# Kernel tuning notes

Hardware: AMD Instinct MI355X
Metric: run time of the kernel (lower is better)

Reference implementation:

```python
import jax, jax.numpy as jnp
import numpy as np

T, INP, HID, OUT = 32768, 1024, 1024, 7


def setup_inputs() -> dict:
    key = jax.random.key(0)
    ks = jax.random.split(key, 7)
    s_i = 1.0 / np.sqrt(INP)
    s_h = 1.0 / np.sqrt(2 * HID)
    s_o = 1.0 / np.sqrt(HID)
    return {
        "uterance": jax.random.normal(ks[0], (T, INP), dtype=jnp.float32),
        "Wi": jax.random.uniform(ks[1], (HID, INP), jnp.float32, -s_i, s_i),
        "bi": jax.random.uniform(ks[2], (HID,), jnp.float32, -s_i, s_i),
        "Wh": jax.random.uniform(ks[3], (HID, 2 * HID), jnp.float32, -s_h, s_h),
        "bh": jax.random.uniform(ks[4], (HID,), jnp.float32, -s_h, s_h),
        "Wo": jax.random.uniform(ks[5], (OUT, HID), jnp.float32, -s_o, s_o),
        "bo": jax.random.uniform(ks[6], (OUT,), jnp.float32, -s_o, s_o),
    }


def reference(uterance, Wi, bi, Wh, bh, Wo, bo):
    # Input projection is independent of the recurrence -> batch it once.
    # hidden_cur[t] = tanh(i2h(x_t)), shape [T, HID]
    hc_all = jnp.tanh(uterance @ Wi.T + bi)
    # Split h2h weight by the concat halves: combined = [prev, cur]
    Wh_prev = Wh[:, :HID]   # acts on hidden_prev
    Wh_cur = Wh[:, HID:]    # acts on hidden_cur
    # Precompute the cur-half contribution in one GEMM.
    cur_contrib = hc_all @ Wh_cur.T + bh  # [T, HID]

    def step(hidden_prev, cur_c):
        hp = jnp.tanh(hidden_prev @ Wh_prev.T + cur_c)  # [HID]
        pred = jax.nn.softmax(hp @ Wo.T + bo)           # [OUT]
        return hp, pred

    h0 = jnp.zeros((HID,), dtype=uterance.dtype)
    _, preds = jax.lax.scan(step, h0, cur_contrib)
    return jnp.mean(preds, axis=0)  # preds summed over T then / T
```

## Files before the change

### kernel.cpp

```cpp
#include <hip/hip_runtime.h>
#include <cstdint>
#include <cstddef>

#define T_N    32768
#define INP_N  1024
#define HID_N  1024
#define OUT_N  7

template<bool TANH>
__global__ __launch_bounds__(256)
void gemm_bt(const float* __restrict__ A, int lda,
             const float* __restrict__ B, int ldb,
             const float* __restrict__ bias,
             float* __restrict__ C, int N, int K)
{
  __shared__ __align__(16) float As[16][128];
  __shared__ __align__(16) float Bs[16][128];

  const int tid = threadIdx.x;
  const int bm0 = blockIdx.y * 128;
  const int bn0 = blockIdx.x * 128;
  const int tx  = tid & 15;
  const int ty  = tid >> 4;
  const int lm  = tid >> 1;
  const int kq  = (tid & 1) * 8;

  float acc[8][8];
#pragma unroll
  for (int i = 0; i < 8; ++i)
#pragma unroll
    for (int j = 0; j < 8; ++j) acc[i][j] = 0.f;

  const float* Arow = A + (size_t)(bm0 + lm) * lda + kq;
  const float* Brow = B + (size_t)(bn0 + lm) * ldb + kq;

  for (int k0 = 0; k0 < K; k0 += 16) {
    float4 va = *(const float4*)(Arow + k0);
    float4 vb = *(const float4*)(Arow + k0 + 4);
    float4 wa = *(const float4*)(Brow + k0);
    float4 wb = *(const float4*)(Brow + k0 + 4);
    __syncthreads();
    As[kq+0][lm]=va.x; As[kq+1][lm]=va.y; As[kq+2][lm]=va.z; As[kq+3][lm]=va.w;
    As[kq+4][lm]=vb.x; As[kq+5][lm]=vb.y; As[kq+6][lm]=vb.z; As[kq+7][lm]=vb.w;
    Bs[kq+0][lm]=wa.x; Bs[kq+1][lm]=wa.y; Bs[kq+2][lm]=wa.z; Bs[kq+3][lm]=wa.w;
    Bs[kq+4][lm]=wb.x; Bs[kq+5][lm]=wb.y; Bs[kq+6][lm]=wb.z; Bs[kq+7][lm]=wb.w;
    __syncthreads();
#pragma unroll
    for (int kk = 0; kk < 16; ++kk) {
      float4 a0 = *(const float4*)&As[kk][ty*8];
      float4 a1 = *(const float4*)&As[kk][ty*8+4];
      float4 b0 = *(const float4*)&Bs[kk][tx*8];
      float4 b1 = *(const float4*)&Bs[kk][tx*8+4];
      float av[8] = {a0.x,a0.y,a0.z,a0.w,a1.x,a1.y,a1.z,a1.w};
      float bv[8] = {b0.x,b0.y,b0.z,b0.w,b1.x,b1.y,b1.z,b1.w};
#pragma unroll
      for (int i = 0; i < 8; ++i)
#pragma unroll
        for (int j = 0; j < 8; ++j)
          acc[i][j] = fmaf(av[i], bv[j], acc[i][j]);
    }
  }

  float bv[8];
#pragma unroll
  for (int j = 0; j < 8; ++j) bv[j] = bias[bn0 + tx*8 + j];

#pragma unroll
  for (int i = 0; i < 8; ++i) {
    float vo[8];
#pragma unroll
    for (int j = 0; j < 8; ++j) {
      float v = acc[i][j] + bv[j];
      vo[j] = TANH ? tanhf(v) : v;
    }
    float4 o0 = make_float4(vo[0],vo[1],vo[2],vo[3]);
    float4 o1 = make_float4(vo[4],vo[5],vo[6],vo[7]);
    float* cp = &C[(size_t)(bm0 + ty*8 + i) * N + bn0 + tx*8];
    *(float4*)cp = o0;
    *(float4*)(cp + 4) = o1;
  }
}

#define SCAN_G     32
#define SCAN_WGSZ  512
#define SCAN_WAVES 8
#define ROWS_WG    32

__global__ __launch_bounds__(SCAN_WGSZ)
void scan_kernel(const float* __restrict__ Wh,
                 const float* __restrict__ cc,
                 float* __restrict__ hist)
{
  const int g   = blockIdx.x;
  const int tid = threadIdx.x;
  const int wv  = tid >> 6;
  const int ln  = tid & 63;
  const int r   = ln & 31;
  const int h2  = ln >> 5;
  const int row = g * ROWS_WG + r;
  const int colbase = wv * 128 + h2 * 64;

  __shared__ __align__(16) float hseg[SCAN_WAVES * 128];
  __shared__ float part[2][16][ROWS_WG];

  float4 wreg[16];
  {
    const float* wp = Wh + (size_t)row * (2 * HID_N) + colbase;
#pragma unroll
    for (int q = 0; q < 16; ++q) wreg[q] = *(const float4*)(wp + 4*q);
  }

  float ccp = 0.f;
  if (ln < ROWS_WG) ccp = cc[(size_t)wv * HID_N + g * ROWS_WG + ln];

  uint32_t* histu = (uint32_t*)hist;

  for (int t = 0; t < T_N; ++t) {
    float a, b;
    if (t > 0) {
      const uint32_t* src = histu + (size_t)(t - 1) * HID_N + wv * 128;
      uint32_t au, bu;
      for (;;) {
        au = __hip_atomic_load(src + ln,      __ATOMIC_RELAXED, __HIP_MEMORY_SCOPE_AGENT);
        bu = __hip_atomic_load(src + 64 + ln, __ATOMIC_RELAXED, __HIP_MEMORY_SCOPE_AGENT);
        if (__all((au != 0xFFFFFFFFu) && (bu != 0xFFFFFFFFu))) break;
      }
      a = __uint_as_float(au);
      b = __uint_as_float(bu);
    } else {
      a = 0.f; b = 0.f;
    }

    hseg[wv*128 + ln]      = a;
    hseg[wv*128 + 64 + ln] = b;

    float p0 = 0.f, p1 = 0.f, p2 = 0.f, p3 = 0.f;
#pragma unroll
    for (int q = 0; q < 16; ++q) {
      float4 h4 = *(const float4*)&hseg[colbase + q*4];
      p0 = fmaf(wreg[q].x, h4.x, p0);
      p1 = fmaf(wreg[q].y, h4.y, p1);
      p2 = fmaf(wreg[q].z, h4.z, p2);
      p3 = fmaf(wreg[q].w, h4.w, p3);
    }
    part[t & 1][wv*2 + h2][r] = (p0 + p1) + (p2 + p3);
    __syncthreads();

    if (wv == (t & 7)) {
      if (ln < ROWS_WG) {
        float s = 0.f;
#pragma unroll
        for (int idx = 0; idx < 16; ++idx) s += part[t & 1][idx][ln];
        float val = tanhf(s + ccp);
        __hip_atomic_store(histu + (size_t)t * HID_N + g * ROWS_WG + ln,
                           __float_as_uint(val),
                           __ATOMIC_RELAXED, __HIP_MEMORY_SCOPE_AGENT);
        int tn = t + SCAN_WAVES;
        ccp = (tn < T_N) ? cc[(size_t)tn * HID_N + g * ROWS_WG + ln] : 0.f;
      }
    }
  }
}

__global__ __launch_bounds__(256)
void out_kernel(const float* __restrict__ hist,
                const float* __restrict__ Wo,
                const float* __restrict__ bo,
                float* __restrict__ out)
{
  const int wv = threadIdx.x >> 6;
  const int ln = threadIdx.x & 63;
  const int gw = blockIdx.x * 4 + wv;
  const int nw = gridDim.x * 4;

  float bor[OUT_N];
#pragma unroll
  for (int o = 0; o < OUT_N; ++o) bor[o] = bo[o];

  float acc[OUT_N];
#pragma unroll
  for (int o = 0; o < OUT_N; ++o) acc[o] = 0.f;

  for (int t = gw; t < T_N; t += nw) {
    const float* hrow = hist + (size_t)t * HID_N + ln * 16;
    float4 h0 = *(const float4*)(hrow);
    float4 h1 = *(const float4*)(hrow + 4);
    float4 h2 = *(const float4*)(hrow + 8);
    float4 h3 = *(const float4*)(hrow + 12);

    float z[OUT_N];
#pragma unroll
    for (int o = 0; o < OUT_N; ++o) {
      const float* wrow = Wo + (size_t)o * HID_N + ln * 16;
      float4 w0 = *(const float4*)(wrow);
      float4 w1 = *(const float4*)(wrow + 4);
      float4 w2 = *(const float4*)(wrow + 8);
      float4 w3 = *(const float4*)(wrow + 12);
      float s;
      s  = h0.x*w0.x + h0.y*w0.y + h0.z*w0.z + h0.w*w0.w;
      s += h1.x*w1.x + h1.y*w1.y + h1.z*w1.z + h1.w*w1.w;
      s += h2.x*w2.x + h2.y*w2.y + h2.z*w2.z + h2.w*w2.w;
      s += h3.x*w3.x + h3.y*w3.y + h3.z*w3.z + h3.w*w3.w;
      z[o] = s;
    }
#pragma unroll
    for (int o = 0; o < OUT_N; ++o) {
#pragma unroll
      for (int off = 1; off < 64; off <<= 1)
        z[o] += __shfl_xor(z[o], off);
      z[o] += bor[o];
    }
    float m = z[0];
#pragma unroll
    for (int o = 1; o < OUT_N; ++o) m = fmaxf(m, z[o]);
    float e[OUT_N], s = 0.f;
#pragma unroll
    for (int o = 0; o < OUT_N; ++o) { e[o] = expf(z[o] - m); s += e[o]; }
    float inv = 1.f / s;
#pragma unroll
    for (int o = 0; o < OUT_N; ++o) acc[o] = fmaf(e[o], inv, acc[o]);
  }

  if (ln == 0) {
#pragma unroll
    for (int o = 0; o < OUT_N; ++o)
      atomicAdd(&out[o], acc[o] * (1.0f / (float)T_N));
  }
}

extern "C" void kernel_launch(void* const* d_in, const int* in_sizes, int n_in,
                              void* d_out, int out_size, void* d_ws, size_t ws_size,
                              hipStream_t stream)
{
  const float* U  = (const float*)d_in[0];
  const float* Wi = (const float*)d_in[1];
  const float* bi = (const float*)d_in[2];
  const float* Wh = (const float*)d_in[3];
  const float* bh = (const float*)d_in[4];
  const float* Wo = (const float*)d_in[5];
  const float* bo = (const float*)d_in[6];
  float* out = (float*)d_out;

  const size_t mat = (size_t)T_N * HID_N;
  float* hc = (float*)d_ws;
  float* cc = hc + mat;
  float* hist = hc;

  dim3 gg(HID_N / 128, T_N / 128);

  gemm_bt<true ><<<gg, 256, 0, stream>>>(U,  INP_N, Wi, INP_N, bi, hc, HID_N, INP_N);
  gemm_bt<false><<<gg, 256, 0, stream>>>(hc, HID_N, Wh + HID_N, 2 * HID_N, bh, cc, HID_N, HID_N);
  hipMemsetAsync(hist, 0xFF, mat * sizeof(float), stream);
  scan_kernel<<<SCAN_G, SCAN_WGSZ, 0, stream>>>(Wh, cc, hist);
  hipMemsetAsync(out, 0, OUT_N * sizeof(float), stream);
  out_kernel<<<1024, 256, 0, stream>>>(hist, Wo, bo, out);
}
```

Baseline: 54.08 ms.

## Use tagged 64-bit ring mailbox for scan handoff instead of full sentinel memset

The recurrent scan now publishes each hidden value in a small ring buffer of 64-bit packets that carry the step index as a tag. Readers poll the tag rather than a 0xFF sentinel, so only the ring has to be memset instead of the whole T×HID history, which is now written separately with nontemporal stores. A fallback path (used when the workspace is too small) polls packed 64-bit sentinel pairs. The change also uses a fast exp/rcp tanh, a tree reduction of the partial sums, nontemporal cc prefetch, and a launch_bounds occupancy hint. Costs are a wider polling load per lane, a 16-step ring that depends on producers never running that far ahead, and less accurate tanh.

```diff
diff --git a/kernel.cpp b/kernel.cpp
--- a/kernel.cpp
+++ b/kernel.cpp
@@ -6,6 +6,8 @@
 #define INP_N  1024
 #define HID_N  1024
 #define OUT_N  7
+#define SENT   0xFFFFFFFFu
+#define RING   16
 
 template<bool TANH>
 __global__ __launch_bounds__(256)
@@ -83,13 +85,14 @@
 
 #define SCAN_G     32
 #define SCAN_WGSZ  512
-#define SCAN_WAVES 8
 #define ROWS_WG    32
 
-__global__ __launch_bounds__(SCAN_WGSZ)
+template<bool TAGGED>
+__global__ __launch_bounds__(SCAN_WGSZ, 2)
 void scan_kernel(const float* __restrict__ Wh,
                  const float* __restrict__ cc,
-                 float* __restrict__ hist)
+                 float* __restrict__ hist,
+                 void* __restrict__ mb_)
 {
   const int g   = blockIdx.x;
   const int tid = threadIdx.x;
@@ -100,8 +103,11 @@
   const int row = g * ROWS_WG + r;
   const int colbase = wv * 128 + h2 * 64;
 
-  __shared__ __align__(16) float hseg[SCAN_WAVES * 128];
+  __shared__ __align__(16) float hseg[8 * 128];
   __shared__ float part[2][16][ROWS_WG];
+
+  uint64_t* mb64 = (uint64_t*)mb_;
+  uint32_t* mb32 = (uint32_t*)mb_;
 
   float4 wreg[16];
   {
@@ -113,26 +119,35 @@
   float ccp = 0.f;
   if (ln < ROWS_WG) ccp = cc[(size_t)wv * HID_N + g * ROWS_WG + ln];
 
-  uint32_t* histu = (uint32_t*)hist;
-
   for (int t = 0; t < T_N; ++t) {
-    float a, b;
     if (t > 0) {
-      const uint32_t* src = histu + (size_t)(t - 1) * HID_N + wv * 128;
-      uint32_t au, bu;
-      for (;;) {
-        au = __hip_atomic_load(src + ln,      __ATOMIC_RELAXED, __HIP_MEMORY_SCOPE_AGENT);
-        bu = __hip_atomic_load(src + 64 + ln, __ATOMIC_RELAXED, __HIP_MEMORY_SCOPE_AGENT);
-        if (__all((au != 0xFFFFFFFFu) && (bu != 0xFFFFFFFFu))) break;
+      if (TAGGED) {
+        const uint64_t* src =
+            mb64 + (size_t)((t - 1) & (RING - 1)) * HID_N + wv * 128;
+        const uint32_t want = (uint32_t)(t - 1);
+        uint64_t v0, v1;
+        for (;;) {
+          v0 = __hip_atomic_load(src + 2*ln,     __ATOMIC_RELAXED, __HIP_MEMORY_SCOPE_AGENT);
+          v1 = __hip_atomic_load(src + 2*ln + 1, __ATOMIC_RELAXED, __HIP_MEMORY_SCOPE_AGENT);
+          if (__all(((uint32_t)(v0 >> 32) == want) & ((uint32_t)(v1 >> 32) == want))) break;
+        }
+        hseg[wv*128 + 2*ln]     = __uint_as_float((uint32_t)v0);
+        hseg[wv*128 + 2*ln + 1] = __uint_as_float((uint32_t)v1);
+      } else {
+        const uint64_t* src =
+            (const uint64_t*)(mb32 + (size_t)(t - 1) * HID_N + wv * 128);
+        uint64_t v;
+        for (;;) {
+          v = __hip_atomic_load(src + ln, __ATOMIC_RELAXED, __HIP_MEMORY_SCOPE_AGENT);
+          if (__all(((uint32_t)v != SENT) && ((uint32_t)(v >> 32) != SENT))) break;
+        }
+        hseg[wv*128 + 2*ln]     = __uint_as_float((uint32_t)v);
+        hseg[wv*128 + 2*ln + 1] = __uint_as_float((uint32_t)(v >> 32));
       }
-      a = __uint_as_float(au);
-      b = __uint_as_float(bu);
     } else {
-      a = 0.f; b = 0.f;
-    }
-
-    hseg[wv*128 + ln]      = a;
-    hseg[wv*128 + 64 + ln] = b;
+      hseg[wv*128 + 2*ln]     = 0.f;
+      hseg[wv*128 + 2*ln + 1] = 0.f;
+    }
 
     float p0 = 0.f, p1 = 0.f, p2 = 0.f, p3 = 0.f;
 #pragma unroll
@@ -146,18 +161,31 @@
     part[t & 1][wv*2 + h2][r] = (p0 + p1) + (p2 + p3);
     __syncthreads();
 
-    if (wv == (t & 7)) {
-      if (ln < ROWS_WG) {
-        float s = 0.f;
-#pragma unroll
-        for (int idx = 0; idx < 16; ++idx) s += part[t & 1][idx][ln];
-        float val = tanhf(s + ccp);
-        __hip_atomic_store(histu + (size_t)t * HID_N + g * ROWS_WG + ln,
+    if (wv == (t & 7) && ln < ROWS_WG) {
+      float s[16];
+#pragma unroll
+      for (int i = 0; i < 16; ++i) s[i] = part[t & 1][i][ln];
+#pragma unroll
+      for (int d = 8; d > 0; d >>= 1)
+#pragma unroll
+        for (int i = 0; i < d; ++i) s[i] += s[i + d];
+      float x = s[0] + ccp;
+      float ex  = __expf(2.0f * x);
+      float val = 1.0f - 2.0f * __builtin_amdgcn_rcpf(ex + 1.0f);
+
+      if (TAGGED) {
+        uint64_t pkt = ((uint64_t)(uint32_t)t << 32) | (uint64_t)__float_as_uint(val);
+        __hip_atomic_store(mb64 + (size_t)(t & (RING - 1)) * HID_N + g * ROWS_WG + ln,
+                           pkt, __ATOMIC_RELAXED, __HIP_MEMORY_SCOPE_AGENT);
+        __builtin_nontemporal_store(val, hist + (size_t)t * HID_N + g * ROWS_WG + ln);
+      } else {
+        __hip_atomic_store(mb32 + (size_t)t * HID_N + g * ROWS_WG + ln,
                            __float_as_uint(val),
                            __ATOMIC_RELAXED, __HIP_MEMORY_SCOPE_AGENT);
-        int tn = t + SCAN_WAVES;
-        ccp = (tn < T_N) ? cc[(size_t)tn * HID_N + g * ROWS_WG + ln] : 0.f;
       }
+      int tn = t + 8;
+      if (tn < T_N)
+        ccp = __builtin_nontemporal_load(cc + (size_t)tn * HID_N + g * ROWS_WG + ln);
     }
   }
 }
@@ -242,16 +270,26 @@
   float* out = (float*)d_out;
 
   const size_t mat = (size_t)T_N * HID_N;
-  float* hc = (float*)d_ws;
-  float* cc = hc + mat;
+  float* hc   = (float*)d_ws;
+  float* cc   = hc + mat;
   float* hist = hc;
+
+  const size_t mb_bytes = (size_t)RING * HID_N * sizeof(uint64_t);
+  const size_t need     = 2 * mat * sizeof(float) + mb_bytes;
+  const bool tagged     = (ws_size >= need);
+  void* mb = tagged ? (void*)(cc + mat) : (void*)hist;
 
   dim3 gg(HID_N / 128, T_N / 128);
 
   gemm_bt<true ><<<gg, 256, 0, stream>>>(U,  INP_N, Wi, INP_N, bi, hc, HID_N, INP_N);
   gemm_bt<false><<<gg, 256, 0, stream>>>(hc, HID_N, Wh + HID_N, 2 * HID_N, bh, cc, HID_N, HID_N);
-  hipMemsetAsync(hist, 0xFF, mat * sizeof(float), stream);
-  scan_kernel<<<SCAN_G, SCAN_WGSZ, 0, stream>>>(Wh, cc, hist);
+  if (tagged) {
+    hipMemsetAsync(mb, 0xFF, mb_bytes, stream);
+    scan_kernel<true ><<<SCAN_G, SCAN_WGSZ, 0, stream>>>(Wh, cc, hist, mb);
+  } else {
+    hipMemsetAsync(mb, 0xFF, mat * sizeof(float), stream);
+    scan_kernel<false><<<SCAN_G, SCAN_WGSZ, 0, stream>>>(Wh, cc, hist, mb);
+  }
   hipMemsetAsync(out, 0, OUT_N * sizeof(float), stream);
   out_kernel<<<1024, 256, 0, stream>>>(hist, Wo, bo, out);
 }
```

Measured after the change: 47.00 ms. 13.1% less time.
